# Performance work log

Hardware: AMD Instinct MI355X
Metric: run time of the kernel (lower is better)

The kernel has to match this reference:

```python
import jax, jax.numpy as jnp
import numpy as np

B, N, F = 32, 1024, 64          # batch, total nodes, local_cnn_dims
P, n, m, e = 8, 128, 256, 1024  # partitions, nodes/part, neighbors/part, edges/part
EF, T, H, W, G, R, L2 = 8, 16, 128, 8, 128, 256, 128


def leaky(z, s):
    return jnp.where(z >= 0, z, s * z)


def setup_inputs() -> dict:
    key = jax.random.key(0)
    ks = jax.random.split(key, 32)
    s = 0.05
    return {
        "x": jax.random.normal(ks[0], (B, N, F), jnp.float32),
        "t": jax.random.normal(ks[1], (B, T), jnp.float32),
        "ef": jax.random.normal(ks[2], (P, e, EF + 1), jnp.float32),
        "linc": jax.random.uniform(ks[3], (P, n, e), jnp.float32) / 32.0,
        "rinc": jax.random.uniform(ks[4], (P, e, m), jnp.float32) / 16.0,
        "cap": jax.random.normal(ks[5], (P, n), jnp.float32),
        "k1_w": jax.random.normal(ks[6], (P, H, EF), jnp.float32) * s,
        "k1_b": jax.random.normal(ks[7], (P, H), jnp.float32) * s,
        "k2_w": jax.random.normal(ks[8], (P, H, T), jnp.float32) * s,
        "k3_w": jax.random.normal(ks[9], (P, H, F), jnp.float32) * s,
        "k4_w": jax.random.normal(ks[10], (P, H, F), jnp.float32) * s,
        "k5_w": jax.random.normal(ks[11], (P, W, H), jnp.float32) * s,
        "k5_b": jax.random.normal(ks[12], (P, W), jnp.float32) * s,
        "gc_w": jax.random.normal(ks[13], (P, G, W * F), jnp.float32) * s,
        "gc_b": jax.random.normal(ks[14], (P, G), jnp.float32) * s,
        "r0_w": jax.random.normal(ks[15], (P, R, G * n), jnp.float32) * 0.005,
        "r1_w": jax.random.normal(ks[16], (P, R, T), jnp.float32) * s,
        "r1_b": jax.random.normal(ks[17], (P, R), jnp.float32) * s,
        "r2_w": jax.random.normal(ks[18], (P, R, n), jnp.float32) * s,
        "r3_w": jax.random.normal(ks[19], (P, n, R), jnp.float32) * s,
        "r3_b": jax.random.normal(ks[20], (P, n), jnp.float32) * s,
        "conv_w": jax.random.normal(ks[21], (L2, G, P), jnp.float32) * s,
        "conv_b": jax.random.normal(ks[22], (L2,), jnp.float32) * s,
        "nodes_idx": jax.random.randint(ks[23], (P, n), 0, N),
        "nbr_idx": jax.random.randint(ks[24], (P, m), 0, N),
    }


def reference(x, t, ef, linc, rinc, cap,
              k1_w, k1_b, k2_w, k3_w, k4_w, k5_w, k5_b, gc_w, gc_b,
              r0_w, r1_w, r1_b, r2_w, r3_w, r3_b, conv_w, conv_b,
              nodes_idx, nbr_idx):
    # gather node subsets per partition
    xg = x[:, nodes_idx]                                   # [B,P,n,F]
    xn = x[:, nbr_idx]                                     # [B,P,m,F]
    rx = jnp.einsum('pem,bpmf->bpef', rinc, xn)            # rinc @ x[nbrs]
    lx = jnp.einsum('pne,bpnf->bpef', linc, xg)            # linc^T @ x[nodes]
    # edge-conditioned kernel
    k = (jnp.einsum('phc,pec->peh', k1_w, ef[..., :-1]) + k1_b[:, None, :])[None]
    k = k + jnp.einsum('pht,bt->bph', k2_w, t)[:, :, None, :]
    k = k + jnp.einsum('phf,bpef->bpeh', k3_w, lx)
    k = k + jnp.einsum('phf,bpef->bpeh', k4_w, rx)
    kernel = jax.nn.relu(jnp.einsum('pwh,bpeh->bpew', k5_w, leaky(k, 0.02))
                         + k5_b[:, None, :])               # [B,P,e,W]
    # message passing: linc @ (kernel * rx) over edges
    y = jnp.einsum('pne,bpew,bpef->bpnwf', linc, kernel, rx)  # [B,P,n,W,F]
    y = y.reshape(B, P, n, W * F)
    y = jax.nn.relu(jnp.einsum('pgk,bpnk->bpng', gc_w, y) + gc_b[:, None, :])
    # readout weights per node
    h = (jnp.einsum('prk,bpk->bpr', r0_w, y.reshape(B, P, n * G))
         + jnp.einsum('prt,bt->bpr', r1_w, t) + r1_b[None]
         + jnp.einsum('prn,pn->pr', r2_w, cap)[None])
    w = jax.nn.relu(jnp.einsum('pnr,bpr->bpn', r3_w, leaky(h, 0.01)) + r3_b[None])
    res = jnp.einsum('bpn,bpng->bpg', w, y)                # [B,P,G]
    # conv1d with kernel_size=P collapses partition axis
    out = leaky(jnp.einsum('lgp,bpg->bl', conv_w, res) + conv_b, 0.02)
    return out  # [B, L2]
```

## Files before the change

### kernel.cpp

```cpp
#include <hip/hip_runtime.h>
#include <math.h>

#define B_ 32
#define N_ 1024
#define F_ 64
#define P_ 8
#define n_ 128
#define m_ 256
#define e_ 1024
#define EF_ 8
#define T_ 16
#define H_ 128
#define W_ 8
#define G_ 128
#define R_ 256
#define L2_ 128

typedef unsigned short u16;
typedef unsigned int u32;
typedef __attribute__((ext_vector_type(8))) short bf16x8;
typedef __attribute__((ext_vector_type(4))) float f32x4;

__device__ __forceinline__ float leakyf(float z, float s) { return z >= 0.f ? z : s * z; }

__device__ __forceinline__ u16 f2bf(float f) {
    u32 u = __float_as_uint(f);
    u += 0x7FFFu + ((u >> 16) & 1u);
    return (u16)(u >> 16);
}
__device__ __forceinline__ float bf2f(u16 h) { return __uint_as_float(((u32)h) << 16); }
__device__ __forceinline__ u32 pk(float a, float b) { return (u32)f2bf(a) | ((u32)f2bf(b) << 16); }

__device__ __forceinline__ int swz64(int r, int c) {
    return r * 64 + ((((c >> 2) ^ ((r >> 3) & 15)) << 2) | (c & 3));
}
__device__ __forceinline__ float4 ld64(const float* lds, int r, int c4) {
    return *reinterpret_cast<const float4*>(lds + r * 64 + ((c4 ^ ((r >> 3) & 15)) << 2));
}

__device__ __forceinline__ int swzi(int row, int col) {
    return row * 64 + ((((col >> 3) ^ (row & 7)) << 3) | (col & 7));
}
__device__ __forceinline__ bf16x8 ldfrag(const u16* lds, int row, int kb) {
    return *reinterpret_cast<const bf16x8*>(lds + row * 64 + ((((kb >> 3) ^ (row & 7)) << 3)));
}
__device__ __forceinline__ int swzi128(int row, int col) {
    return row * 128 + ((((col >> 3) ^ (row & 7)) << 3) | (col & 7));
}
__device__ __forceinline__ bf16x8 ldfrag128(const u16* lds, int row, int kb) {
    return *reinterpret_cast<const bf16x8*>(lds + row * 128 + ((((kb >> 3) ^ (row & 7)) << 3)));
}

__global__ __launch_bounds__(256) void k_prep(const float* __restrict__ linc,
                                              const float* __restrict__ rinc,
                                              const float* __restrict__ gcw,
                                              u16* __restrict__ lincbf,
                                              u16* __restrict__ rincbf,
                                              u16* __restrict__ gcwbf) {
    int i = blockIdx.x * 256 + threadIdx.x;
    const float* src;
    u16* dst;
    int base;
    if (i < 262144) { src = linc; dst = lincbf; base = 0; }
    else if (i < 786432) { src = rinc; dst = rincbf; base = 262144; }
    else { src = gcw; dst = gcwbf; base = 786432; }
    int j = i - base;
    float4 v = reinterpret_cast<const float4*>(src)[j];
    ushort4 o = make_ushort4(f2bf(v.x), f2bf(v.y), f2bf(v.z), f2bf(v.w));
    reinterpret_cast<ushort4*>(dst)[j] = o;
}

__global__ __launch_bounds__(256) void k_prep2(const float* __restrict__ linc,
                                               const float* __restrict__ k4w,
                                               const float* __restrict__ k1w,
                                               const float* __restrict__ k2w,
                                               const float* __restrict__ k1b,
                                               const float* __restrict__ ef,
                                               const float* __restrict__ k5w,
                                               u16* __restrict__ lincT,
                                               u16* __restrict__ Bw,
                                               u16* __restrict__ efb,
                                               u16* __restrict__ k5wb) {
    const int blk = blockIdx.x, t = threadIdx.x;
    if (blk < 64) {
        const int p = blk >> 3, et = blk & 7, e0 = et * 128;
        __shared__ u16 S[128 * 128];
        {
            const int nn = t >> 1, seg = (t & 1) * 64;
            const float4* src = reinterpret_cast<const float4*>(
                linc + (size_t)(p * n_ + nn) * e_ + e0 + seg);
#pragma unroll
            for (int q = 0; q < 16; q += 2) {
                float4 a = src[q], b2 = src[q + 1];
                uint4 o = make_uint4(pk(a.x, a.y), pk(a.z, a.w), pk(b2.x, b2.y), pk(b2.z, b2.w));
                int colbase = seg + q * 4;
                int ch = (colbase >> 3) ^ (nn & 7);
                *reinterpret_cast<uint4*>(S + nn * 128 + ch * 8) = o;
            }
        }
        __syncthreads();
        {
            const int e = t >> 1, ns = (t & 1) * 64;
            u16* dst = lincT + ((size_t)(p * e_) + e0 + e) * n_ + ns;
#pragma unroll
            for (int q = 0; q < 8; q++) {
                u16 v[8];
#pragma unroll
                for (int k = 0; k < 8; k++) v[k] = S[swzi128(ns + q * 8 + k, e)];
                uint4 o = make_uint4((u32)v[0] | ((u32)v[1] << 16), (u32)v[2] | ((u32)v[3] << 16),
                                     (u32)v[4] | ((u32)v[5] << 16), (u32)v[6] | ((u32)v[7] << 16));
                *reinterpret_cast<uint4*>(dst + q * 8) = o;
            }
        }
    } else if (blk < 68) {
        int flat = (blk - 64) * 256 + t;
        int p = flat >> 7, h = flat & 127;
        u16* dst = Bw + (size_t)flat * 128;
        const float4* s4 = reinterpret_cast<const float4*>(k4w + (size_t)(p * H_ + h) * F_);
#pragma unroll
        for (int q = 0; q < 16; q += 2) {
            float4 a = s4[q], b2 = s4[q + 1];
            *reinterpret_cast<uint4*>(dst + q * 4) =
                make_uint4(pk(a.x, a.y), pk(a.z, a.w), pk(b2.x, b2.y), pk(b2.z, b2.w));
        }
        {
            const float4* s1 = reinterpret_cast<const float4*>(k1w + (size_t)(p * H_ + h) * EF_);
            float4 a = s1[0], b2 = s1[1];
            *reinterpret_cast<uint4*>(dst + 64) =
                make_uint4(pk(a.x, a.y), pk(a.z, a.w), pk(b2.x, b2.y), pk(b2.z, b2.w));
        }
        {
            const float4* s2 = reinterpret_cast<const float4*>(k2w + (size_t)(p * H_ + h) * T_);
#pragma unroll
            for (int q = 0; q < 4; q += 2) {
                float4 a = s2[q], b2 = s2[q + 1];
                *reinterpret_cast<uint4*>(dst + 72 + q * 4) =
                    make_uint4(pk(a.x, a.y), pk(a.z, a.w), pk(b2.x, b2.y), pk(b2.z, b2.w));
            }
        }
        *reinterpret_cast<uint4*>(dst + 88) = make_uint4((u32)f2bf(k1b[p * H_ + h]), 0, 0, 0);
        *reinterpret_cast<uint4*>(dst + 96) = make_uint4(0, 0, 0, 0);
        *reinterpret_cast<uint4*>(dst + 104) = make_uint4(0, 0, 0, 0);
        *reinterpret_cast<uint4*>(dst + 112) = make_uint4(0, 0, 0, 0);
        *reinterpret_cast<uint4*>(dst + 120) = make_uint4(0, 0, 0, 0);
    } else if (blk < 100) {
        int flat = (blk - 68) * 256 + t;
        const float* s = ef + (size_t)flat * (EF_ + 1);
        float v0 = s[0], v1 = s[1], v2 = s[2], v3 = s[3], v4 = s[4], v5 = s[5], v6 = s[6], v7 = s[7];
        *reinterpret_cast<uint4*>(efb + (size_t)flat * 8) =
            make_uint4(pk(v0, v1), pk(v2, v3), pk(v4, v5), pk(v6, v7));
    } else {
        int p = blk - 100;
        int row = t >> 4, col8 = (t & 15) * 8;
        uint4 o = make_uint4(0, 0, 0, 0);
        if (row < 8) {
            const float4* s = reinterpret_cast<const float4*>(k5w + (size_t)(p * W_ + row) * H_ + col8);
            float4 a = s[0], b2 = s[1];
            o = make_uint4(pk(a.x, a.y), pk(a.z, a.w), pk(b2.x, b2.y), pk(b2.z, b2.w));
        }
        int ch = (col8 >> 3) ^ (row & 7);
        *reinterpret_cast<uint4*>(k5wb + (size_t)p * 2048 + row * 128 + ch * 8) = o;
    }
}

__global__ __launch_bounds__(256) void k_rx(const float* __restrict__ x,
                                            const u16* __restrict__ rincbf,
                                            const int* __restrict__ nbr,
                                            u16* __restrict__ rxbf) {
    const int et = blockIdx.x, p = blockIdx.y, b = blockIdx.z;
    const int t = threadIdx.x, lane = t & 63, wid = t >> 6;
    __shared__ __align__(16) u16 A_lds[128 * 64];
    __shared__ __align__(16) u16 BT_lds[64 * 64];
    f32x4 acc[2][4];
#pragma unroll
    for (int i = 0; i < 2; i++)
#pragma unroll
        for (int j = 0; j < 4; j++) acc[i][j] = 0.f;

    const int e0 = et * 128;
    for (int c = 0; c < 4; c++) {
        const int m0 = c * 64;
        __syncthreads();
        {
            int ee = t >> 1, seg = t & 1;
            const uint4* src = reinterpret_cast<const uint4*>(
                rincbf + ((size_t)(p * e_ + e0 + ee) * m_ + m0 + seg * 32));
#pragma unroll
            for (int q = 0; q < 4; q++) {
                uint4 v = src[q];
                int ch = (seg * 4 + q) ^ (ee & 7);
                *reinterpret_cast<uint4*>(A_lds + ee * 64 + ch * 8) = v;
            }
        }
        {
            int mm = t >> 2, fq = (t & 3) * 16;
            int row = nbr[p * m_ + m0 + mm];
            const float4* sx = reinterpret_cast<const float4*>(
                x + (size_t)(b * N_ + row) * F_ + fq);
#pragma unroll
            for (int q = 0; q < 4; q++) {
                float4 v = sx[q];
                int f0 = fq + q * 4;
                BT_lds[swzi(f0 + 0, mm)] = f2bf(v.x);
                BT_lds[swzi(f0 + 1, mm)] = f2bf(v.y);
                BT_lds[swzi(f0 + 2, mm)] = f2bf(v.z);
                BT_lds[swzi(f0 + 3, mm)] = f2bf(v.w);
            }
        }
        __syncthreads();
        const int wm0 = wid * 32, r15 = lane & 15, g4 = lane >> 4;
#pragma unroll
        for (int ks = 0; ks < 2; ks++) {
            int kb = ks * 32 + g4 * 8;
            bf16x8 af[2], bfr[4];
#pragma unroll
            for (int mf = 0; mf < 2; mf++) af[mf] = ldfrag(A_lds, wm0 + mf * 16 + r15, kb);
#pragma unroll
            for (int nf = 0; nf < 4; nf++) bfr[nf] = ldfrag(BT_lds, nf * 16 + r15, kb);
#pragma unroll
            for (int mf = 0; mf < 2; mf++)
#pragma unroll
                for (int nf = 0; nf < 4; nf++)
                    acc[mf][nf] = __builtin_amdgcn_mfma_f32_16x16x32_bf16(af[mf], bfr[nf], acc[mf][nf], 0, 0, 0);
        }
    }
    const int r15 = lane & 15, g4 = lane >> 4;
#pragma unroll
    for (int mf = 0; mf < 2; mf++)
#pragma unroll
        for (int nf = 0; nf < 4; nf++)
#pragma unroll
            for (int r = 0; r < 4; r++) {
                int erow = e0 + wid * 32 + mf * 16 + g4 * 4 + r;
                int f = nf * 16 + r15;
                rxbf[((size_t)(b * P_ + p) * e_ + erow) * F_ + f] = f2bf(acc[mf][nf][r]);
            }
}

__global__ __launch_bounds__(256) void k_u(const float* __restrict__ x,
                                           const float* __restrict__ k3w,
                                           const int* __restrict__ nodes,
                                           u16* __restrict__ uT) {
    const int p = blockIdx.x, b = blockIdx.y;
    const int t = threadIdx.x;
    const int th = t & 15;
    const int tn = t >> 4;
    __shared__ float xg[128 * 64];
    __shared__ float kw[128 * 64];
    for (int idx = t; idx < 8192; idx += 256) {
        int r = idx >> 6, f = idx & 63;
        int row = nodes[p * n_ + r];
        xg[swz64(r, f)] = x[(size_t)(b * N_ + row) * F_ + f];
        kw[swz64(r, f)] = k3w[(size_t)(p * H_ + r) * F_ + f];
    }
    __syncthreads();
    float acc[8][8];
#pragma unroll
    for (int i = 0; i < 8; i++)
#pragma unroll
        for (int j = 0; j < 8; j++) acc[i][j] = 0.f;
#pragma unroll 2
    for (int k4 = 0; k4 < 16; k4++) {
        float4 xv[8];
#pragma unroll
        for (int i = 0; i < 8; i++) xv[i] = ld64(xg, tn * 8 + i, k4);
#pragma unroll
        for (int j = 0; j < 8; j++) {
            float4 kv = ld64(kw, th * 8 + j, k4);
#pragma unroll
            for (int i = 0; i < 8; i++) {
                acc[i][j] += xv[i].x * kv.x + xv[i].y * kv.y + xv[i].z * kv.z + xv[i].w * kv.w;
            }
        }
    }
#pragma unroll
    for (int j = 0; j < 8; j++) {
        uint4 o = make_uint4(pk(acc[0][j], acc[1][j]), pk(acc[2][j], acc[3][j]),
                             pk(acc[4][j], acc[5][j]), pk(acc[6][j], acc[7][j]));
        *reinterpret_cast<uint4*>(uT + ((size_t)(b * P_ + p) * H_ + th * 8 + j) * n_ + tn * 8) = o;
    }
}

__global__ __launch_bounds__(256) void k_kern(const u16* __restrict__ lincT,
                                              const u16* __restrict__ uT,
                                              const u16* __restrict__ rxbf,
                                              const u16* __restrict__ Bw,
                                              const u16* __restrict__ efb,
                                              const float* __restrict__ tin,
                                              const u16* __restrict__ k5wb,
                                              const float* __restrict__ k5b,
                                              float* __restrict__ kern) {
    const int et = blockIdx.x, p = blockIdx.y, b = blockIdx.z;
    const int t = threadIdx.x, lane = t & 63, wid = t >> 6;
    const int r15 = lane & 15, g4 = lane >> 4;
    const int wm = (wid >> 1) * 64, wn = (wid & 1) * 64;
    __shared__ __align__(16) u16 S[128 * 128 + 16 * 128];
    u16* A_lds = S;
    u16* B_lds = S + 8192;
    u16* k5l = S + 16384;

    {
        uint4 v = reinterpret_cast<const uint4*>(k5wb + (size_t)p * 2048)[t];
        reinterpret_cast<uint4*>(k5l)[t] = v;
    }
    uint4 tinlo, tinhi;
    {
        const float4* s = reinterpret_cast<const float4*>(tin + b * T_);
        float4 a = s[0], b2 = s[1], c2 = s[2], d2 = s[3];
        tinlo = make_uint4(pk(a.x, a.y), pk(a.z, a.w), pk(b2.x, b2.y), pk(b2.z, b2.w));
        tinhi = make_uint4(pk(c2.x, c2.y), pk(c2.z, c2.w), pk(d2.x, d2.y), pk(d2.z, d2.w));
    }

    f32x4 acc[4][4];
#pragma unroll
    for (int i = 0; i < 4; i++)
#pragma unroll
        for (int j = 0; j < 4; j++) acc[i][j] = 0.f;

    const int e0 = et * 128;
    const size_t pb_e = (size_t)(b * P_ + p) * e_;
    const int row = t >> 1, half = t & 1;

    for (int c = 0; c < 4; c++) {
        __syncthreads();
        if (c < 2) {
            const uint4* src = reinterpret_cast<const uint4*>(
                lincT + ((size_t)(p * e_) + e0 + row) * n_ + c * 64 + half * 32);
#pragma unroll
            for (int q = 0; q < 4; q++) {
                uint4 v = src[q];
                int ch = (half * 4 + q) ^ (row & 7);
                *reinterpret_cast<uint4*>(A_lds + row * 64 + ch * 8) = v;
            }
        } else if (c == 2) {
            const uint4* src = reinterpret_cast<const uint4*>(
                rxbf + (pb_e + e0 + row) * F_ + half * 32);
#pragma unroll
            for (int q = 0; q < 4; q++) {
                uint4 v = src[q];
                int ch = (half * 4 + q) ^ (row & 7);
                *reinterpret_cast<uint4*>(A_lds + row * 64 + ch * 8) = v;
            }
        } else {
            uint4 w[4];
            if (half == 0) {
                w[0] = *reinterpret_cast<const uint4*>(efb + ((size_t)(p * e_) + e0 + row) * 8);
                w[1] = tinlo;
                w[2] = tinhi;
                w[3] = make_uint4(0x00003F80u, 0, 0, 0);
            } else {
                w[0] = w[1] = w[2] = w[3] = make_uint4(0, 0, 0, 0);
            }
#pragma unroll
            for (int q = 0; q < 4; q++) {
                int ch = (half * 4 + q) ^ (row & 7);
                *reinterpret_cast<uint4*>(A_lds + row * 64 + ch * 8) = w[q];
            }
        }
        {
            const uint4* src;
            if (c < 2)
                src = reinterpret_cast<const uint4*>(
                    uT + ((size_t)(b * P_ + p) * H_ + row) * n_ + c * 64 + half * 32);
            else
                src = reinterpret_cast<const uint4*>(
                    Bw + (size_t)(p * H_ + row) * 128 + (c - 2) * 64 + half * 32);
#pragma unroll
            for (int q = 0; q < 4; q++) {
                uint4 v = src[q];
                int ch = (half * 4 + q) ^ (row & 7);
                *reinterpret_cast<uint4*>(B_lds + row * 64 + ch * 8) = v;
            }
        }
        __syncthreads();
#pragma unroll
        for (int ks = 0; ks < 2; ks++) {
            int kb = ks * 32 + g4 * 8;
            bf16x8 af[4], bfr[4];
#pragma unroll
            for (int mf = 0; mf < 4; mf++) af[mf] = ldfrag(A_lds, wm + mf * 16 + r15, kb);
#pragma unroll
            for (int nf = 0; nf < 4; nf++) bfr[nf] = ldfrag(B_lds, wn + nf * 16 + r15, kb);
#pragma unroll
            for (int mf = 0; mf < 4; mf++)
#pragma unroll
                for (int nf = 0; nf < 4; nf++)
                    acc[mf][nf] = __builtin_amdgcn_mfma_f32_16x16x32_bf16(af[mf], bfr[nf], acc[mf][nf], 0, 0, 0);
        }
    }
    __syncthreads();
    u16* Kl = S;
#pragma unroll
    for (int mf = 0; mf < 4; mf++)
#pragma unroll
        for (int nf = 0; nf < 4; nf++)
#pragma unroll
            for (int r = 0; r < 4; r++) {
                int er = wm + mf * 16 + g4 * 4 + r;
                int hc = wn + nf * 16 + r15;
                Kl[swzi128(er, hc)] = f2bf(leakyf(acc[mf][nf][r], 0.02f));
            }
    __syncthreads();
    f32x4 acc2[2];
    acc2[0] = 0.f;
    acc2[1] = 0.f;
#pragma unroll
    for (int ks = 0; ks < 4; ks++) {
        int kb = ks * 32 + g4 * 8;
        bf16x8 bf5 = ldfrag128(k5l, r15, kb);
#pragma unroll
        for (int mf2 = 0; mf2 < 2; mf2++) {
            bf16x8 af = ldfrag128(Kl, wid * 32 + mf2 * 16 + r15, kb);
            acc2[mf2] = __builtin_amdgcn_mfma_f32_16x16x32_bf16(af, bf5, acc2[mf2], 0, 0, 0);
        }
    }
    if (r15 < 8) {
        float kb5 = k5b[p * W_ + r15];
#pragma unroll
        for (int mf2 = 0; mf2 < 2; mf2++)
#pragma unroll
            for (int r = 0; r < 4; r++) {
                int er = e0 + wid * 32 + mf2 * 16 + g4 * 4 + r;
                kern[(pb_e + er) * W_ + r15] = fmaxf(acc2[mf2][r] + kb5, 0.f);
            }
    }
}

__global__ __launch_bounds__(256) void k_q(const u16* __restrict__ rxbf,
                                           const float* __restrict__ kernb,
                                           const u16* __restrict__ gcwbf,
                                           u16* __restrict__ QTbf) {
    const int et = blockIdx.x, p = blockIdx.y, b = blockIdx.z;
    const int t = threadIdx.x, lane = t & 63, wid = t >> 6;
    const int r15 = lane & 15, g4 = lane >> 4;
    const int wm = (wid >> 1) * 32, wn = (wid & 1) * 64;
    __shared__ __align__(16) u16 RX[64 * 64];
    __shared__ __align__(16) u16 GW[2][128 * 64];
    __shared__ float KL[8 * 64];

    const int e0 = et * 64;
    const size_t pb_e = (size_t)(b * P_ + p) * e_;

    {
        int rr = t >> 2, sg = t & 3;
        const uint4* src = reinterpret_cast<const uint4*>(rxbf + (pb_e + e0 + rr) * F_ + sg * 16);
#pragma unroll
        for (int q = 0; q < 2; q++) {
            uint4 v = src[q];
            int ch = (sg * 2 + q) ^ (rr & 7);
            *reinterpret_cast<uint4*>(RX + rr * 64 + ch * 8) = v;
        }
        if (t < 128) {
            int row = t >> 1, half = t & 1;
            float4 kv = *reinterpret_cast<const float4*>(kernb + (pb_e + e0 + row) * W_ + half * 4);
            KL[(half * 4 + 0) * 64 + row] = kv.x;
            KL[(half * 4 + 1) * 64 + row] = kv.y;
            KL[(half * 4 + 2) * 64 + row] = kv.z;
            KL[(half * 4 + 3) * 64 + row] = kv.w;
        }
        int gg = t >> 1, seg = t & 1;
        const uint4* gsrc = reinterpret_cast<const uint4*>(
            gcwbf + (size_t)(p * G_ + gg) * 512 + seg * 32);
#pragma unroll
        for (int q = 0; q < 4; q++) {
            uint4 v = gsrc[q];
            int ch = (seg * 4 + q) ^ (gg & 7);
            *reinterpret_cast<uint4*>(GW[0] + gg * 64 + ch * 8) = v;
        }
    }
    __syncthreads();

    f32x4 acc[2][4];
#pragma unroll
    for (int i = 0; i < 2; i++)
#pragma unroll
        for (int j = 0; j < 4; j++) acc[i][j] = 0.f;

    bf16x8 af[2][2];
#pragma unroll
    for (int mf = 0; mf < 2; mf++)
#pragma unroll
        for (int ks = 0; ks < 2; ks++)
            af[mf][ks] = ldfrag(RX, wm + mf * 16 + r15, ks * 32 + g4 * 8);

    const f32x4 zero = 0.f;
    const int gg = t >> 1, seg = t & 1;
    for (int w = 0; w < 8; w++) {
        const int cur = w & 1;
        if (w < 7) {
            const uint4* gsrc = reinterpret_cast<const uint4*>(
                gcwbf + (size_t)(p * G_ + gg) * 512 + (w + 1) * 64 + seg * 32);
#pragma unroll
            for (int q = 0; q < 4; q++) {
                uint4 v = gsrc[q];
                int ch = (seg * 4 + q) ^ (gg & 7);
                *reinterpret_cast<uint4*>(GW[cur ^ 1] + gg * 64 + ch * 8) = v;
            }
        }
        f32x4 kk[2];
#pragma unroll
        for (int mf = 0; mf < 2; mf++)
            kk[mf] = *reinterpret_cast<const f32x4*>(KL + w * 64 + wm + mf * 16 + g4 * 4);
#pragma unroll
        for (int nf = 0; nf < 4; nf++) {
            bf16x8 b0 = ldfrag(GW[cur], wn + nf * 16 + r15, g4 * 8);
            bf16x8 b1 = ldfrag(GW[cur], wn + nf * 16 + r15, 32 + g4 * 8);
#pragma unroll
            for (int mf = 0; mf < 2; mf++) {
                f32x4 macc = __builtin_amdgcn_mfma_f32_16x16x32_bf16(af[mf][0], b0, zero, 0, 0, 0);
                macc = __builtin_amdgcn_mfma_f32_16x16x32_bf16(af[mf][1], b1, macc, 0, 0, 0);
                acc[mf][nf] += kk[mf] * macc;
            }
        }
        __syncthreads();
    }
#pragma unroll
    for (int mf = 0; mf < 2; mf++)
#pragma unroll
        for (int nf = 0; nf < 4; nf++) {
            int g = wn + nf * 16 + r15;
            int er = e0 + wm + mf * 16 + g4 * 4;
            ushort4 o = make_ushort4(f2bf(acc[mf][nf][0]), f2bf(acc[mf][nf][1]),
                                     f2bf(acc[mf][nf][2]), f2bf(acc[mf][nf][3]));
            *reinterpret_cast<ushort4*>(QTbf + ((size_t)(b * P_ + p) * G_ + g) * e_ + er) = o;
        }
}

__global__ __launch_bounds__(256) void k_y2(const u16* __restrict__ lincbf,
                                            const u16* __restrict__ QTbf,
                                            const float* __restrict__ gcb,
                                            float* __restrict__ y2) {
    const int p = blockIdx.x, b = blockIdx.y;
    const int t = threadIdx.x, lane = t & 63, wid = t >> 6;
    __shared__ __align__(16) u16 A_lds[128 * 64];
    __shared__ __align__(16) u16 BT_lds[128 * 64];
    f32x4 acc[4][4];
#pragma unroll
    for (int i = 0; i < 4; i++)
#pragma unroll
        for (int j = 0; j < 4; j++) acc[i][j] = 0.f;

    const size_t pb_g = (size_t)(b * P_ + p) * G_;
    const int wm = (wid >> 1) * 64, wn = (wid & 1) * 64;
    const int r15 = lane & 15, g4 = lane >> 4;

    for (int c = 0; c < 16; c++) {
        const int e0 = c * 64;
        __syncthreads();
        {
            int nn = t >> 1, seg = t & 1;
            const uint4* src = reinterpret_cast<const uint4*>(
                lincbf + (size_t)(p * n_ + nn) * e_ + e0 + seg * 32);
#pragma unroll
            for (int q = 0; q < 4; q++) {
                uint4 v = src[q];
                int ch = (seg * 4 + q) ^ (nn & 7);
                *reinterpret_cast<uint4*>(A_lds + nn * 64 + ch * 8) = v;
            }
        }
        {
            int gg = t >> 1, seg = t & 1;
            const uint4* src = reinterpret_cast<const uint4*>(
                QTbf + (pb_g + gg) * e_ + e0 + seg * 32);
#pragma unroll
            for (int q = 0; q < 4; q++) {
                uint4 v = src[q];
                int ch = (seg * 4 + q) ^ (gg & 7);
                *reinterpret_cast<uint4*>(BT_lds + gg * 64 + ch * 8) = v;
            }
        }
        __syncthreads();
#pragma unroll
        for (int ks = 0; ks < 2; ks++) {
            int kb = ks * 32 + g4 * 8;
            bf16x8 af[4], bfr[4];
#pragma unroll
            for (int mf = 0; mf < 4; mf++) af[mf] = ldfrag(A_lds, wm + mf * 16 + r15, kb);
#pragma unroll
            for (int nf = 0; nf < 4; nf++) bfr[nf] = ldfrag(BT_lds, wn + nf * 16 + r15, kb);
#pragma unroll
            for (int mf = 0; mf < 4; mf++)
#pragma unroll
                for (int nf = 0; nf < 4; nf++)
                    acc[mf][nf] = __builtin_amdgcn_mfma_f32_16x16x32_bf16(af[mf], bfr[nf], acc[mf][nf], 0, 0, 0);
        }
    }
#pragma unroll
    for (int mf = 0; mf < 4; mf++)
#pragma unroll
        for (int nf = 0; nf < 4; nf++) {
            int g = wn + nf * 16 + r15;
            float gb = gcb[p * G_ + g];
#pragma unroll
            for (int r = 0; r < 4; r++) {
                int nrow = wm + mf * 16 + g4 * 4 + r;
                y2[((size_t)(b * P_ + p) * n_ + nrow) * G_ + g] = fmaxf(acc[mf][nf][r] + gb, 0.f);
            }
        }
}

__global__ __launch_bounds__(256) void k_h1(const float* __restrict__ r0w,
                                            const float* __restrict__ y2,
                                            float* __restrict__ hpart) {
    const int ks = blockIdx.x;
    const int rt = blockIdx.y;
    const int p  = blockIdx.z;
    const int t = threadIdx.x, lane = t & 63, wid = t >> 6;
    const int r15 = lane & 15, g4 = lane >> 4;
    __shared__ __align__(16) u16 A_lds[64 * 128];
    __shared__ __align__(16) u16 B_lds[32 * 128];
    const int kc = ks * 512;
    const int row0 = rt * 64;

    f32x4 acc[2];
    acc[0] = 0.f;
    acc[1] = 0.f;

    const int sar = t >> 2, sas = t & 3;
    const int sbb = t >> 3, sbs = t & 7;

    for (int it = 0; it < 4; it++) {
        __syncthreads();
        {
            const float4* src = reinterpret_cast<const float4*>(
                r0w + ((size_t)(p * R_) + row0 + sar) * 16384 + kc + it * 128 + sas * 32);
#pragma unroll
            for (int q = 0; q < 4; q++) {
                float4 a = src[q * 2], b2 = src[q * 2 + 1];
                uint4 o = make_uint4(pk(a.x, a.y), pk(a.z, a.w), pk(b2.x, b2.y), pk(b2.z, b2.w));
                int ch = (sas * 4 + q) ^ (sar & 7);
                *reinterpret_cast<uint4*>(A_lds + sar * 128 + ch * 8) = o;
            }
        }
        {
            const float4* src = reinterpret_cast<const float4*>(
                y2 + (size_t)(sbb * P_ + p) * 16384 + kc + it * 128 + sbs * 16);
            float4 a = src[0], b2 = src[1], c2 = src[2], d2 = src[3];
            uint4 o0 = make_uint4(pk(a.x, a.y), pk(a.z, a.w), pk(b2.x, b2.y), pk(b2.z, b2.w));
            uint4 o1 = make_uint4(pk(c2.x, c2.y), pk(c2.z, c2.w), pk(d2.x, d2.y), pk(d2.z, d2.w));
            int ch0 = (sbs * 2) ^ (sbb & 7);
            int ch1 = (sbs * 2 + 1) ^ (sbb & 7);
            *reinterpret_cast<uint4*>(B_lds + sbb * 128 + ch0 * 8) = o0;
            *reinterpret_cast<uint4*>(B_lds + sbb * 128 + ch1 * 8) = o1;
        }
        __syncthreads();
#pragma unroll
        for (int ksl = 0; ksl < 4; ksl++) {
            int kb = ksl * 32 + g4 * 8;
            bf16x8 af = ldfrag128(A_lds, wid * 16 + r15, kb);
#pragma unroll
            for (int nf = 0; nf < 2; nf++) {
                bf16x8 bfr = ldfrag128(B_lds, nf * 16 + r15, kb);
                acc[nf] = __builtin_amdgcn_mfma_f32_16x16x32_bf16(af, bfr, acc[nf], 0, 0, 0);
            }
        }
    }
#pragma unroll
    for (int nf = 0; nf < 2; nf++) {
        int b = nf * 16 + r15;
        int r = row0 + wid * 16 + g4 * 4;
        float4 v = make_float4(acc[nf][0], acc[nf][1], acc[nf][2], acc[nf][3]);
        *reinterpret_cast<float4*>(hpart + (((size_t)(ks * P_ + p) * 32 + b) * 256 + r)) = v;
    }
}

__global__ __launch_bounds__(128) void k_wres(const float* __restrict__ hpart,
                                              const float* __restrict__ r1w,
                                              const float* __restrict__ r1b,
                                              const float* __restrict__ r2w,
                                              const float* __restrict__ cap,
                                              const float* __restrict__ tin,
                                              const float* __restrict__ r3w,
                                              const float* __restrict__ r3b,
                                              const float* __restrict__ y2,
                                              float* __restrict__ res) {
    const int p = blockIdx.x, b = blockIdx.y;
    const int t = threadIdx.x;
    __shared__ float lh[256];
    __shared__ float wl[128];
    for (int rr = t; rr < 256; rr += 128) {
        float s = 0.f;
        for (int ks = 0; ks < 32; ks++)
            s += hpart[(((size_t)(ks * P_ + p) * 32 + b) * 256) + rr];
        for (int tt = 0; tt < T_; tt++) s += r1w[(size_t)(p * R_ + rr) * T_ + tt] * tin[b * T_ + tt];
        s += r1b[p * R_ + rr];
        for (int nn = 0; nn < n_; nn++) s += r2w[(size_t)(p * R_ + rr) * n_ + nn] * cap[p * n_ + nn];
        lh[rr] = leakyf(s, 0.01f);
    }
    __syncthreads();
    {
        const int nn = t;
        float accw = r3b[p * n_ + nn];
        const float* r3p = r3w + (size_t)(p * n_ + nn) * R_;
        for (int r = 0; r < 256; r += 4) {
            float4 rv = *reinterpret_cast<const float4*>(r3p + r);
            accw += rv.x * lh[r] + rv.y * lh[r + 1] + rv.z * lh[r + 2] + rv.w * lh[r + 3];
        }
        wl[nn] = fmaxf(accw, 0.f);
    }
    __syncthreads();
    {
        const int g = t;
        float a = 0.f;
        for (int nn = 0; nn < n_; nn++) a += wl[nn] * y2[((size_t)(b * P_ + p) * n_ + nn) * G_ + g];
        res[(b * P_ + p) * G_ + g] = a;
    }
}

__global__ __launch_bounds__(128) void k_out(const float* __restrict__ convw,
                                             const float* __restrict__ convb,
                                             const float* __restrict__ res,
                                             float* __restrict__ out) {
    const int b = blockIdx.x;
    const int t = threadIdx.x;
    __shared__ float rl[1024];
    for (int idx = t; idx < 1024; idx += 128) rl[idx] = res[b * 1024 + idx];
    __syncthreads();
    float a = convb[t];
    const float* cw = convw + (size_t)t * 1024;
    for (int gp = 0; gp < 1024; gp += 4) {
        float4 v = *reinterpret_cast<const float4*>(cw + gp);
        a += v.x * rl[((gp + 0) & 7) * 128 + ((gp + 0) >> 3)];
        a += v.y * rl[((gp + 1) & 7) * 128 + ((gp + 1) >> 3)];
        a += v.z * rl[((gp + 2) & 7) * 128 + ((gp + 2) >> 3)];
        a += v.w * rl[((gp + 3) & 7) * 128 + ((gp + 3) >> 3)];
    }
    out[b * L2_ + t] = leakyf(a, 0.02f);
}

extern "C" void kernel_launch(void* const* d_in, const int* in_sizes, int n_in,
                              void* d_out, int out_size, void* d_ws, size_t ws_size,
                              hipStream_t stream) {
    const float* x    = (const float*)d_in[0];
    const float* tin  = (const float*)d_in[1];
    const float* ef   = (const float*)d_in[2];
    const float* linc = (const float*)d_in[3];
    const float* rinc = (const float*)d_in[4];
    const float* cap  = (const float*)d_in[5];
    const float* k1w  = (const float*)d_in[6];
    const float* k1b  = (const float*)d_in[7];
    const float* k2w  = (const float*)d_in[8];
    const float* k3w  = (const float*)d_in[9];
    const float* k4w  = (const float*)d_in[10];
    const float* k5w  = (const float*)d_in[11];
    const float* k5b  = (const float*)d_in[12];
    const float* gcw  = (const float*)d_in[13];
    const float* gcb  = (const float*)d_in[14];
    const float* r0w  = (const float*)d_in[15];
    const float* r1w  = (const float*)d_in[16];
    const float* r1b  = (const float*)d_in[17];
    const float* r2w  = (const float*)d_in[18];
    const float* r3w  = (const float*)d_in[19];
    const float* r3b  = (const float*)d_in[20];
    const float* convw = (const float*)d_in[21];
    const float* convb = (const float*)d_in[22];
    const int* nodes  = (const int*)d_in[23];
    const int* nbr    = (const int*)d_in[24];
    float* out = (float*)d_out;

    float* ws = (float*)d_ws;
    u16*   rxbf   = (u16*)ws;
    u16*   uTbf   = (u16*)(ws + 8388608);
    float* kernb  = ws + 10485760;
    u16*   QTbf   = (u16*)(ws + 12582912);
    float* y2b    = ws + 29360128;
    u16*   lincbf = (u16*)(ws + 33554432);
    u16*   lincT  = (u16*)(ws + 34078720);
    u16*   rincbf = (u16*)(ws + 34603008);
    u16*   gcwbf  = (u16*)(ws + 35651584);
    u16*   Bwbf   = (u16*)(ws + 35913728);
    u16*   efbf   = (u16*)(ws + 35979264);
    u16*   k5wbf  = (u16*)(ws + 36012032);
    float* hpart  = ws;
    float* resb   = ws + 10485760;

    k_prep <<<3584, 256, 0, stream>>>(linc, rinc, gcw, lincbf, rincbf, gcwbf);
    k_prep2<<<108, 256, 0, stream>>>(linc, k4w, k1w, k2w, k1b, ef, k5w, lincT, Bwbf, efbf, k5wbf);
    k_rx  <<<dim3(8, P_, B_), 256, 0, stream>>>(x, rincbf, nbr, rxbf);
    k_u   <<<dim3(P_, B_),    256, 0, stream>>>(x, k3w, nodes, uTbf);
    k_kern<<<dim3(8, P_, B_), 256, 0, stream>>>(lincT, uTbf, rxbf, Bwbf, efbf, tin, k5wbf, k5b, kernb);
    k_q   <<<dim3(16, P_, B_), 256, 0, stream>>>(rxbf, kernb, gcwbf, QTbf);
    k_y2  <<<dim3(P_, B_),    256, 0, stream>>>(lincbf, QTbf, gcb, y2b);
    k_h1  <<<dim3(32, 4, P_), 256, 0, stream>>>(r0w, y2b, hpart);
    k_wres<<<dim3(P_, B_),    128, 0, stream>>>(hpart, r1w, r1b, r2w, cap, tin, r3w, r3b, y2b, resb);
    k_out <<<B_, 128, 0, stream>>>(convw, convb, resb, out);
}
```

Measured before the change: 298.4 us.

## Pre-scale rx by kernel weights into LDS and accumulate directly in MFMA

k_q now builds a per-edge bf16 operand of kernel[w]*rx[f] (512 wide) in shared memory, so the gc_w contraction becomes a single K=512 MFMA accumulation instead of per-w MFMA pairs followed by a scalar-weighted vector add. The edge tile shrinks from 64 to 32 rows, which doubles the grid, and each wave now covers a 32x32 output tile. This drops the extra FMA and zero-initialised MFMA chains. In exchange, the kernel*rx product is rounded to bf16 before the MFMA, which adds precision loss, and LDS use grows.

```diff
diff --git a/kernel.cpp b/kernel.cpp
--- a/kernel.cpp
+++ b/kernel.cpp
@@ -49,6 +49,9 @@
 }
 __device__ __forceinline__ bf16x8 ldfrag128(const u16* lds, int row, int kb) {
     return *reinterpret_cast<const bf16x8*>(lds + row * 128 + ((((kb >> 3) ^ (row & 7)) << 3)));
+}
+__device__ __forceinline__ bf16x8 ldfrag512(const u16* lds, int row, int kb) {
+    return *reinterpret_cast<const bf16x8*>(lds + row * 512 + ((((kb >> 3) ^ (row & 7)) << 3)));
 }
 
 __global__ __launch_bounds__(256) void k_prep(const float* __restrict__ linc,
@@ -433,32 +436,34 @@
     const int et = blockIdx.x, p = blockIdx.y, b = blockIdx.z;
     const int t = threadIdx.x, lane = t & 63, wid = t >> 6;
     const int r15 = lane & 15, g4 = lane >> 4;
-    const int wm = (wid >> 1) * 32, wn = (wid & 1) * 64;
-    __shared__ __align__(16) u16 RX[64 * 64];
+    const int wn = wid * 32;
+    __shared__ __align__(16) u16 BP[32 * 512];
     __shared__ __align__(16) u16 GW[2][128 * 64];
-    __shared__ float KL[8 * 64];
-
-    const int e0 = et * 64;
+    const int e0 = et * 32;
     const size_t pb_e = (size_t)(b * P_ + p) * e_;
 
     {
-        int rr = t >> 2, sg = t & 3;
-        const uint4* src = reinterpret_cast<const uint4*>(rxbf + (pb_e + e0 + rr) * F_ + sg * 16);
-#pragma unroll
-        for (int q = 0; q < 2; q++) {
+        const int row = t >> 3, w = t & 7;
+        const float ksc = kernb[(pb_e + e0 + row) * W_ + w];
+        const uint4* src = reinterpret_cast<const uint4*>(rxbf + (pb_e + e0 + row) * F_);
+        u16* dstrow = BP + row * 512;
+#pragma unroll
+        for (int q = 0; q < 8; q++) {
             uint4 v = src[q];
-            int ch = (sg * 2 + q) ^ (rr & 7);
-            *reinterpret_cast<uint4*>(RX + rr * 64 + ch * 8) = v;
-        }
-        if (t < 128) {
-            int row = t >> 1, half = t & 1;
-            float4 kv = *reinterpret_cast<const float4*>(kernb + (pb_e + e0 + row) * W_ + half * 4);
-            KL[(half * 4 + 0) * 64 + row] = kv.x;
-            KL[(half * 4 + 1) * 64 + row] = kv.y;
-            KL[(half * 4 + 2) * 64 + row] = kv.z;
-            KL[(half * 4 + 3) * 64 + row] = kv.w;
-        }
-        int gg = t >> 1, seg = t & 1;
+            u32 vv[4] = {v.x, v.y, v.z, v.w};
+            u32 ov[4];
+#pragma unroll
+            for (int q2 = 0; q2 < 4; q2++) {
+                float f0 = bf2f((u16)(vv[q2] & 0xFFFF)) * ksc;
+                float f1 = bf2f((u16)(vv[q2] >> 16)) * ksc;
+                ov[q2] = (u32)f2bf(f0) | ((u32)f2bf(f1) << 16);
+            }
+            int ch = (w * 8 + q) ^ (row & 7);
+            *reinterpret_cast<uint4*>(dstrow + ch * 8) = make_uint4(ov[0], ov[1], ov[2], ov[3]);
+        }
+    }
+    const int gg = t >> 1, seg = t & 1;
+    {
         const uint4* gsrc = reinterpret_cast<const uint4*>(
             gcwbf + (size_t)(p * G_ + gg) * 512 + seg * 32);
 #pragma unroll
@@ -470,26 +475,17 @@
     }
     __syncthreads();
 
-    f32x4 acc[2][4];
+    f32x4 acc[2][2];
 #pragma unroll
     for (int i = 0; i < 2; i++)
 #pragma unroll
-        for (int j = 0; j < 4; j++) acc[i][j] = 0.f;
-
-    bf16x8 af[2][2];
-#pragma unroll
-    for (int mf = 0; mf < 2; mf++)
-#pragma unroll
-        for (int ks = 0; ks < 2; ks++)
-            af[mf][ks] = ldfrag(RX, wm + mf * 16 + r15, ks * 32 + g4 * 8);
-
-    const f32x4 zero = 0.f;
-    const int gg = t >> 1, seg = t & 1;
-    for (int w = 0; w < 8; w++) {
-        const int cur = w & 1;
-        if (w < 7) {
+        for (int j = 0; j < 2; j++) acc[i][j] = 0.f;
+
+    for (int c = 0; c < 8; c++) {
+        const int cur = c & 1;
+        if (c < 7) {
             const uint4* gsrc = reinterpret_cast<const uint4*>(
-                gcwbf + (size_t)(p * G_ + gg) * 512 + (w + 1) * 64 + seg * 32);
+                gcwbf + (size_t)(p * G_ + gg) * 512 + (c + 1) * 64 + seg * 32);
 #pragma unroll
             for (int q = 0; q < 4; q++) {
                 uint4 v = gsrc[q];
@@ -497,29 +493,32 @@
                 *reinterpret_cast<uint4*>(GW[cur ^ 1] + gg * 64 + ch * 8) = v;
             }
         }
-        f32x4 kk[2];
+        bf16x8 af[2][2], bfr[2][2];
 #pragma unroll
         for (int mf = 0; mf < 2; mf++)
-            kk[mf] = *reinterpret_cast<const f32x4*>(KL + w * 64 + wm + mf * 16 + g4 * 4);
-#pragma unroll
-        for (int nf = 0; nf < 4; nf++) {
-            bf16x8 b0 = ldfrag(GW[cur], wn + nf * 16 + r15, g4 * 8);
-            bf16x8 b1 = ldfrag(GW[cur], wn + nf * 16 + r15, 32 + g4 * 8);
-#pragma unroll
-            for (int mf = 0; mf < 2; mf++) {
-                f32x4 macc = __builtin_amdgcn_mfma_f32_16x16x32_bf16(af[mf][0], b0, zero, 0, 0, 0);
-                macc = __builtin_amdgcn_mfma_f32_16x16x32_bf16(af[mf][1], b1, macc, 0, 0, 0);
-                acc[mf][nf] += kk[mf] * macc;
-            }
-        }
+#pragma unroll
+            for (int ks = 0; ks < 2; ks++)
+                af[mf][ks] = ldfrag512(BP, mf * 16 + r15, c * 64 + ks * 32 + g4 * 8);
+#pragma unroll
+        for (int nf = 0; nf < 2; nf++)
+#pragma unroll
+            for (int ks = 0; ks < 2; ks++)
+                bfr[nf][ks] = ldfrag(GW[cur], wn + nf * 16 + r15, ks * 32 + g4 * 8);
+#pragma unroll
+        for (int mf = 0; mf < 2; mf++)
+#pragma unroll
+            for (int nf = 0; nf < 2; nf++)
+#pragma unroll
+                for (int ks = 0; ks < 2; ks++)
+                    acc[mf][nf] = __builtin_amdgcn_mfma_f32_16x16x32_bf16(af[mf][ks], bfr[nf][ks], acc[mf][nf], 0, 0, 0);
         __syncthreads();
     }
 #pragma unroll
     for (int mf = 0; mf < 2; mf++)
 #pragma unroll
-        for (int nf = 0; nf < 4; nf++) {
+        for (int nf = 0; nf < 2; nf++) {
             int g = wn + nf * 16 + r15;
-            int er = e0 + wm + mf * 16 + g4 * 4;
+            int er = e0 + mf * 16 + g4 * 4;
             ushort4 o = make_ushort4(f2bf(acc[mf][nf][0]), f2bf(acc[mf][nf][1]),
                                      f2bf(acc[mf][nf][2]), f2bf(acc[mf][nf][3]));
             *reinterpret_cast<ushort4*>(QTbf + ((size_t)(b * P_ + p) * G_ + g) * e_ + er) = o;
@@ -779,7 +778,7 @@
     k_rx  <<<dim3(8, P_, B_), 256, 0, stream>>>(x, rincbf, nbr, rxbf);
     k_u   <<<dim3(P_, B_),    256, 0, stream>>>(x, k3w, nodes, uTbf);
     k_kern<<<dim3(8, P_, B_), 256, 0, stream>>>(lincT, uTbf, rxbf, Bwbf, efbf, tin, k5wbf, k5b, kernb);
-    k_q   <<<dim3(16, P_, B_), 256, 0, stream>>>(rxbf, kernb, gcwbf, QTbf);
+    k_q   <<<dim3(32, P_, B_), 256, 0, stream>>>(rxbf, kernb, gcwbf, QTbf);
     k_y2  <<<dim3(P_, B_),    256, 0, stream>>>(lincbf, QTbf, gcb, y2b);
     k_h1  <<<dim3(32, 4, P_), 256, 0, stream>>>(r0w, y2b, hpart);
     k_wres<<<dim3(P_, B_),    128, 0, stream>>>(hpart, r1w, r1b, r2w, cap, tin, r3w, r3b, y2b, resb);
```

New measurement: 315.2 us. +5.6%, slower.
